# Kernel tuning notes

Measured on AMD Instinct MI355X. Metric: run time of the kernel, lower is better.

Reference implementation:

```python
import jax, jax.numpy as jnp
import numpy as np

N = 50000          # nodes
E = 800000         # edges (avg degree 16)
F_IN = 128         # node_feat_dim
HEADS = 4
HID = 64           # hidden_dim (per head)
LAT = 64           # latent_dim
N_EC = 8           # num_edge_classes
SLOPE = 0.2        # GATConv default negative_slope


def setup_inputs() -> dict:
    key = jax.random.key(0)
    ks = jax.random.split(key, 20)
    s = 0.05
    inp = {
        "x": jax.random.normal(ks[0], (N, F_IN), jnp.float32),
        "edge_index": jax.random.randint(ks[1], (2, E), 0, N, jnp.int32),
        # conv1: GATConv(F_IN, HID, heads=HEADS)
        "W1": jax.random.normal(ks[2], (F_IN, HEADS * HID), jnp.float32) * s,
        "att_src1": jax.random.normal(ks[3], (HEADS, HID), jnp.float32) * s,
        "att_dst1": jax.random.normal(ks[4], (HEADS, HID), jnp.float32) * s,
        "b1": jnp.zeros((HEADS * HID,), jnp.float32),
        # conv2: GATConv(HEADS*HID, LAT, heads=1)
        "W2": jax.random.normal(ks[5], (HEADS * HID, LAT), jnp.float32) * s,
        "att_src2": jax.random.normal(ks[6], (1, LAT), jnp.float32) * s,
        "att_dst2": jax.random.normal(ks[7], (1, LAT), jnp.float32) * s,
        "b2": jnp.zeros((LAT,), jnp.float32),
        # decode_nodes: Linear(LAT, F_IN)
        "Wn": jax.random.normal(ks[8], (LAT, F_IN), jnp.float32) * s,
        "bn": jnp.zeros((F_IN,), jnp.float32),
        # decode_edges: Linear(2*LAT, HID) -> ReLU -> Linear(HID, N_EC)
        "We1": jax.random.normal(ks[9], (2 * LAT, HID), jnp.float32) * s,
        "be1": jnp.zeros((HID,), jnp.float32),
        "We2": jax.random.normal(ks[10], (HID, N_EC), jnp.float32) * s,
        "be2": jnp.zeros((N_EC,), jnp.float32),
    }
    return inp


def _gat_conv(x, src, dst, W, att_src, att_dst, b, heads, out_ch):
    """PyG-style GATConv: message src->dst, segment-softmax over incoming edges."""
    n = x.shape[0]
    h = (x @ W).reshape(n, heads, out_ch)          # [N, H, C]
    a_s = (h * att_src).sum(-1)                     # [N, H]
    a_d = (h * att_dst).sum(-1)                     # [N, H]
    alpha = jax.nn.leaky_relu(a_s[src] + a_d[dst], SLOPE)   # [E', H]
    amax = jax.ops.segment_max(alpha, dst, num_segments=n)  # stable softmax
    alpha = jnp.exp(alpha - amax[dst])
    denom = jax.ops.segment_sum(alpha, dst, num_segments=n)
    alpha = alpha / (denom[dst] + 1e-16)
    out = jax.ops.segment_sum(h[src] * alpha[:, :, None], dst, num_segments=n)
    return out.reshape(n, heads * out_ch) + b


def reference(x, edge_index, W1, att_src1, att_dst1, b1, W2, att_src2, att_dst2,
              b2, Wn, bn, We1, be1, We2, be2):
    n = x.shape[0]
    loop = jnp.arange(n, dtype=edge_index.dtype)
    # PyG GATConv adds self-loops by default
    src = jnp.concatenate([edge_index[0], loop])
    dst = jnp.concatenate([edge_index[1], loop])

    h = jax.nn.relu(_gat_conv(x, src, dst, W1, att_src1, att_dst1, b1, HEADS, HID))
    z = _gat_conv(h, src, dst, W2, att_src2, att_dst2, b2, 1, LAT)

    recon_x = z @ Wn + bn
    # edge decode uses the ORIGINAL edge_index (no self-loops)
    edge_z = jnp.concatenate([z[edge_index[0]], z[edge_index[1]]], axis=-1)
    recon_edge_logits = jax.nn.relu(edge_z @ We1 + be1) @ We2 + be2
    return (recon_x, recon_edge_logits)
```

## Files before the change

### kernel.cpp

```cpp
#include <hip/hip_runtime.h>

#define N_NODES 50000
#define N_EDGES 800000
#define F_IN    128
#define HEADS   4
#define HID     64
#define LAT     64
#define N_EC    8
#define SLOPE   0.2f
#define NBUCKET 196
#define PLANE   ((size_t)N_NODES * 128)
#define PLANEU  ((size_t)N_NODES * 64)

typedef __attribute__((ext_vector_type(8))) short bf16x8;
typedef __attribute__((ext_vector_type(4))) float f32x4;

__device__ __forceinline__ float lrelu(float x) { return x > 0.f ? x : SLOPE * x; }
__device__ __forceinline__ float4 operator+(float4 a, float4 b) { return make_float4(a.x+b.x, a.y+b.y, a.z+b.z, a.w+b.w); }
__device__ __forceinline__ float4 lrelu4(float4 a) { return make_float4(lrelu(a.x), lrelu(a.y), lrelu(a.z), lrelu(a.w)); }
__device__ __forceinline__ float4 exp4(float4 a) { return make_float4(__expf(a.x), __expf(a.y), __expf(a.z), __expf(a.w)); }

__device__ __forceinline__ unsigned short f2bf(float f) {
    union { float f; unsigned u; } a; a.f = f;
    unsigned r = a.u + 0x7fffu + ((a.u >> 16) & 1u);
    return (unsigned short)(r >> 16);
}
__device__ __forceinline__ unsigned pack2bf(float x, float y) {
    return (unsigned)f2bf(x) | ((unsigned)f2bf(y) << 16);
}
__device__ __forceinline__ float2 bf2f2(unsigned u) {
    union { unsigned q; float f; } a, b;
    a.q = u << 16; b.q = u & 0xffff0000u;
    return make_float2(a.f, b.f);
}

__global__ __launch_bounds__(256) void bucket_count_kernel(const int* __restrict__ ei,
                                                           int* __restrict__ bcnt) {
    __shared__ int h[NBUCKET];
    int tid = threadIdx.x;
    for (int i = tid; i < NBUCKET; i += 256) h[i] = 0;
    __syncthreads();
    int beg = blockIdx.x * 4096;
    int end = min(beg + 4096, N_EDGES);
    for (int e = beg + tid; e < end; e += 256)
        atomicAdd(&h[ei[N_EDGES + e] >> 8], 1);
    __syncthreads();
    for (int i = tid; i < NBUCKET; i += 256)
        if (h[i]) atomicAdd(&bcnt[i], h[i]);
}

__global__ __launch_bounds__(256) void scan_buckets_kernel(const int* __restrict__ bcnt,
                                                           int* __restrict__ bbase,
                                                           int* __restrict__ bcur,
                                                           int* __restrict__ row_start) {
    __shared__ int sh[NBUCKET + 1];
    int tid = threadIdx.x;
    if (tid < NBUCKET) { sh[tid] = bcnt[tid]; bcur[tid] = 0; }
    __syncthreads();
    if (tid == 0) {
        int a = 0;
        for (int i = 0; i < NBUCKET; i++) { int t = sh[i]; sh[i] = a; a += t; }
        sh[NBUCKET] = a;
        row_start[N_NODES] = N_EDGES;
    }
    __syncthreads();
    if (tid <= NBUCKET) bbase[tid] = sh[tid];
}

__global__ __launch_bounds__(256) void coarse_scatter_kernel(const int* __restrict__ ei,
                                                             const int* __restrict__ bbase,
                                                             int* __restrict__ bcur,
                                                             uint2* __restrict__ coarse) {
    __shared__ int h[NBUCKET];
    __shared__ int base[NBUCKET];
    int tid = threadIdx.x;
    for (int i = tid; i < NBUCKET; i += 256) h[i] = 0;
    __syncthreads();
    int beg = blockIdx.x * 4096;
    int w0_[16], o_[16], b_[16];
#pragma unroll
    for (int k = 0; k < 16; k++) {
        int e = beg + k * 256 + tid;
        b_[k] = -1;
        if (e < N_EDGES) {
            int s = ei[e], d = ei[N_EDGES + e];
            int bk = d >> 8;
            b_[k] = bk;
            w0_[k] = s | ((d & 255) << 16);
            o_[k] = e;
            atomicAdd(&h[bk], 1);
        }
    }
    __syncthreads();
    for (int i = tid; i < NBUCKET; i += 256) {
        int c = h[i];
        base[i] = c ? atomicAdd(&bcur[i], c) : 0;
        h[i] = 0;
    }
    __syncthreads();
#pragma unroll
    for (int k = 0; k < 16; k++) {
        if (b_[k] >= 0) {
            int r = atomicAdd(&h[b_[k]], 1);
            coarse[bbase[b_[k]] + base[b_[k]] + r] = make_uint2((unsigned)w0_[k], (unsigned)o_[k]);
        }
    }
}

__global__ __launch_bounds__(256) void fine_pass_kernel(const uint2* __restrict__ coarse,
                                                        const int* __restrict__ bbase,
                                                        const float4* __restrict__ as4,
                                                        const float4* __restrict__ ad4,
                                                        int* __restrict__ esrc,
                                                        float4* __restrict__ alpha4,
                                                        uint2* __restrict__ edges2,
                                                        int* __restrict__ row_start) {
    int bucket = blockIdx.x;
    int tid = threadIdx.x;
    int lo = bbase[bucket], hi = bbase[bucket + 1];
    __shared__ int h[256];
    __shared__ int wsum[4];
    __shared__ int cur[256];
    h[tid] = 0;
    __syncthreads();
    for (int p = lo + tid; p < hi; p += 256)
        atomicAdd(&h[(coarse[p].x >> 16) & 0xff], 1);
    __syncthreads();
    int v = h[tid];
    int lane = tid & 63, w = tid >> 6;
    int incl = v;
#pragma unroll
    for (int off = 1; off < 64; off <<= 1) {
        int t = __shfl_up(incl, off, 64);
        if (lane >= off) incl += t;
    }
    if (lane == 63) wsum[w] = incl;
    __syncthreads();
    if (tid == 0) {
        int a = 0;
#pragma unroll
        for (int i = 0; i < 4; i++) { int t = wsum[i]; wsum[i] = a; a += t; }
    }
    __syncthreads();
    int excl = incl - v + wsum[w];
    int node = bucket * 256 + tid;
    if (node < N_NODES) row_start[node] = lo + excl;
    cur[tid] = lo + excl;
    __syncthreads();
    for (int p = lo + tid; p < hi; p += 256) {
        uint2 r = coarse[p];
        int dl = (r.x >> 16) & 0xff;
        int s = r.x & 0xffff;
        int d = bucket * 256 + dl;
        int pos = atomicAdd(&cur[dl], 1);
        esrc[pos] = s;
        edges2[pos] = make_uint2((unsigned)(s | (d << 16)), r.y);
        alpha4[pos] = exp4(lrelu4(as4[s] + ad4[d]));
    }
}

__global__ void watt_kernel(const float* __restrict__ W1, const float* __restrict__ as_,
                            const float* __restrict__ ad_, float* __restrict__ watt) {
    int idx = blockIdx.x * blockDim.x + threadIdx.x;
    if (idx >= 128 * 8) return;
    int k = idx >> 3, j = idx & 7;
    int h = j & 3;
    const float* av = (j < 4) ? as_ : ad_;
    float sum = 0.f;
    for (int c = 0; c < 64; c++) sum += W1[k * 256 + h * 64 + c] * av[h * 64 + c];
    watt[k * 8 + j] = sum;
}

__global__ void build_wts_kernel(const float* __restrict__ W1, const float* __restrict__ W2,
                                 const float* __restrict__ Wn, const float* __restrict__ We1,
                                 const float* __restrict__ We2,
                                 unsigned short* __restrict__ Bt1, unsigned short* __restrict__ Bt2,
                                 unsigned short* __restrict__ Btd, unsigned short* __restrict__ Bte) {
    int idx = blockIdx.x * blockDim.x + threadIdx.x;
    if (idx < 256 * 128) {
        int n = idx >> 7, k = idx & 127;
        Bt1[idx] = f2bf(W1[k * 256 + n]);
    }
    if (idx < 64 * 256) {
        int n = idx >> 8, k = idx & 255;
        Bt2[idx] = f2bf(W2[k * 64 + n]);
    }
    if (idx < 256 * 64) {
        int n = idx >> 6, k = idx & 63;
        float v;
        if (n < 128) v = Wn[k * 128 + n];
        else {
            int nn = n - 128;
            v = (nn < 64) ? We1[k * 64 + nn] : We1[(64 + k) * 64 + (nn - 64)];
        }
        Btd[idx] = f2bf(v);
    }
    if (idx < 16 * 64) {
        int n = idx >> 6, k = idx & 63;
        Bte[idx] = (n < 8) ? f2bf(We2[k * 8 + n]) : (unsigned short)0;
    }
}

__global__ __launch_bounds__(256) void asad_kernel(const float* __restrict__ x,
                                                   const float* __restrict__ watt,
                                                   float4* __restrict__ as4,
                                                   float4* __restrict__ ad4,
                                                   unsigned* __restrict__ xb) {
    int wid = (blockIdx.x * blockDim.x + threadIdx.x) >> 6;
    int lane = threadIdx.x & 63;
    if (wid >= N_NODES) return;
    float2 xv = *reinterpret_cast<const float2*>(&x[(size_t)wid * 128 + lane * 2]);
    xb[(size_t)wid * 64 + lane] = pack2bf(xv.x, xv.y);
    float p[8];
    const float* w0 = &watt[(2 * lane) * 8];
    const float* w1 = &watt[(2 * lane + 1) * 8];
#pragma unroll
    for (int j = 0; j < 8; j++) p[j] = fmaf(xv.x, w0[j], xv.y * w1[j]);
#pragma unroll
    for (int off = 32; off; off >>= 1)
#pragma unroll
        for (int j = 0; j < 8; j++) p[j] += __shfl_xor(p[j], off, 64);
    if (lane == 0) {
        as4[wid] = make_float4(p[0], p[1], p[2], p[3]);
        ad4[wid] = make_float4(p[4], p[5], p[6], p[7]);
    }
}

__global__ __launch_bounds__(256) void agg4x_acc_kernel(const unsigned short* __restrict__ xb,
                                                        const float4* __restrict__ as4,
                                                        const float4* __restrict__ ad4,
                                                        const int* __restrict__ row_start,
                                                        const int* __restrict__ esrc,
                                                        const float4* __restrict__ alpha4,
                                                        unsigned* __restrict__ xaggb) {
    int wid = (blockIdx.x * blockDim.x + threadIdx.x) >> 6;
    int lane = threadIdx.x & 63;
    if (wid >= N_NODES) return;
    int beg = __builtin_amdgcn_readfirstlane(row_start[wid]);
    int end = __builtin_amdgcn_readfirstlane(row_start[wid + 1]);
    float4 adn = ad4[wid];
    float4 e_self = exp4(lrelu4(as4[wid] + adn));
    float4 den = e_self;
    float2 xv = bf2f2(*reinterpret_cast<const unsigned*>(&xb[(size_t)wid * 128 + lane * 2]));
    float2 acc0 = make_float2(e_self.x * xv.x, e_self.x * xv.y);
    float2 acc1 = make_float2(e_self.y * xv.x, e_self.y * xv.y);
    float2 acc2 = make_float2(e_self.z * xv.x, e_self.z * xv.y);
    float2 acc3 = make_float2(e_self.w * xv.x, e_self.w * xv.y);
    int j = beg;
    for (; j + 1 < end; j += 2) {
        float4 ea = alpha4[j];
        int sa = esrc[j];
        float4 eb = alpha4[j + 1];
        int sb = esrc[j + 1];
        float2 va = bf2f2(*reinterpret_cast<const unsigned*>(&xb[(size_t)sa * 128 + lane * 2]));
        float2 vb = bf2f2(*reinterpret_cast<const unsigned*>(&xb[(size_t)sb * 128 + lane * 2]));
        acc0.x = fmaf(ea.x, va.x, acc0.x); acc0.y = fmaf(ea.x, va.y, acc0.y);
        acc1.x = fmaf(ea.y, va.x, acc1.x); acc1.y = fmaf(ea.y, va.y, acc1.y);
        acc2.x = fmaf(ea.z, va.x, acc2.x); acc2.y = fmaf(ea.z, va.y, acc2.y);
        acc3.x = fmaf(ea.w, va.x, acc3.x); acc3.y = fmaf(ea.w, va.y, acc3.y);
        den = den + ea;
        acc0.x = fmaf(eb.x, vb.x, acc0.x); acc0.y = fmaf(eb.x, vb.y, acc0.y);
        acc1.x = fmaf(eb.y, vb.x, acc1.x); acc1.y = fmaf(eb.y, vb.y, acc1.y);
        acc2.x = fmaf(eb.z, vb.x, acc2.x); acc2.y = fmaf(eb.z, vb.y, acc2.y);
        acc3.x = fmaf(eb.w, vb.x, acc3.x); acc3.y = fmaf(eb.w, vb.y, acc3.y);
        den = den + eb;
    }
    if (j < end) {
        float4 ea = alpha4[j];
        int sa = esrc[j];
        float2 va = bf2f2(*reinterpret_cast<const unsigned*>(&xb[(size_t)sa * 128 + lane * 2]));
        acc0.x = fmaf(ea.x, va.x, acc0.x); acc0.y = fmaf(ea.x, va.y, acc0.y);
        acc1.x = fmaf(ea.y, va.x, acc1.x); acc1.y = fmaf(ea.y, va.y, acc1.y);
        acc2.x = fmaf(ea.z, va.x, acc2.x); acc2.y = fmaf(ea.z, va.y, acc2.y);
        acc3.x = fmaf(ea.w, va.x, acc3.x); acc3.y = fmaf(ea.w, va.y, acc3.y);
        den = den + ea;
    }
    float i0 = 1.f / (den.x + 1e-16f);
    float i1 = 1.f / (den.y + 1e-16f);
    float i2 = 1.f / (den.z + 1e-16f);
    float i3 = 1.f / (den.w + 1e-16f);
    size_t base = (size_t)wid * 64 + lane;
    xaggb[0 * PLANEU + base] = pack2bf(acc0.x * i0, acc0.y * i0);
    xaggb[1 * PLANEU + base] = pack2bf(acc1.x * i1, acc1.y * i1);
    xaggb[2 * PLANEU + base] = pack2bf(acc2.x * i2, acc2.y * i2);
    xaggb[3 * PLANEU + base] = pack2bf(acc3.x * i3, acc3.y * i3);
}


template <int K>
__global__ __launch_bounds__(256) void mfma_gemm1_kernel(const unsigned short* __restrict__ A,
                                                         int lda, long aPlane,
                                                         const unsigned short* __restrict__ Bt,
                                                         const float* __restrict__ bias,
                                                         unsigned short* __restrict__ C, int ldc,
                                                         int M) {
    int tid = threadIdx.x;
    int w = tid >> 6, l = tid & 63;
    int bcol = blockIdx.y * 64;
    A += (size_t)blockIdx.y * aPlane;
    int row_a = blockIdx.x * 64 + w * 16 + (l & 15);
    int kq = (l >> 4) * 8;
    bool aval = row_a < M;
    const unsigned short* Arow = A + (size_t)row_a * lda;
    f32x4 acc[4] = {};
#pragma unroll
    for (int kb = 0; kb < K / 32; kb++) {
        int k0 = kb * 32 + kq;
        bf16x8 a = {};
        if (aval) a = *reinterpret_cast<const bf16x8*>(&Arow[k0]);
#pragma unroll
        for (int nb = 0; nb < 4; nb++) {
            bf16x8 b = *reinterpret_cast<const bf16x8*>(
                &Bt[(size_t)(bcol + nb * 16 + (l & 15)) * K + k0]);
            acc[nb] = __builtin_amdgcn_mfma_f32_16x16x32_bf16(a, b, acc[nb], 0, 0, 0);
        }
    }
    int orow = blockIdx.x * 64 + w * 16 + (l >> 4) * 4;
#pragma unroll
    for (int nb = 0; nb < 4; nb++) {
        int col = bcol + nb * 16 + (l & 15);
        float bb = bias[col];
#pragma unroll
        for (int r = 0; r < 4; r++) {
            int row = orow + r;
            if (row < M) C[(size_t)row * ldc + col] = f2bf(fmaxf(acc[nb][r] + bb, 0.f));
        }
    }
}

__global__ __launch_bounds__(256) void mfma_gemm2_kernel(const unsigned short* __restrict__ A,
                                                         const unsigned short* __restrict__ Bt,
                                                         const float* __restrict__ att_src,
                                                         const float* __restrict__ att_dst,
                                                         unsigned short* __restrict__ h2b,
                                                         float* __restrict__ as_,
                                                         float* __restrict__ ad_, int M) {
    int tid = threadIdx.x;
    int w = tid >> 6, l = tid & 63;
    int row_a = blockIdx.x * 64 + w * 16 + (l & 15);
    int kq = (l >> 4) * 8;
    bool aval = row_a < M;
    const unsigned short* Arow = A + (size_t)row_a * 256;
    f32x4 acc[4] = {};
#pragma unroll
    for (int kb = 0; kb < 8; kb++) {
        int k0 = kb * 32 + kq;
        bf16x8 a = {};
        if (aval) a = *reinterpret_cast<const bf16x8*>(&Arow[k0]);
#pragma unroll
        for (int nb = 0; nb < 4; nb++) {
            bf16x8 b = *reinterpret_cast<const bf16x8*>(
                &Bt[(size_t)(nb * 16 + (l & 15)) * 256 + k0]);
            acc[nb] = __builtin_amdgcn_mfma_f32_16x16x32_bf16(a, b, acc[nb], 0, 0, 0);
        }
    }
    int orow = blockIdx.x * 64 + w * 16 + (l >> 4) * 4;
    float ps[4] = {}, pd[4] = {};
#pragma unroll
    for (int nb = 0; nb < 4; nb++) {
        int col = nb * 16 + (l & 15);
        float s = att_src[col], dd = att_dst[col];
#pragma unroll
        for (int r = 0; r < 4; r++) {
            float v = acc[nb][r];
            ps[r] = fmaf(v, s, ps[r]);
            pd[r] = fmaf(v, dd, pd[r]);
            int row = orow + r;
            if (row < M) h2b[(size_t)row * 64 + col] = f2bf(v);
        }
    }
#pragma unroll
    for (int off = 1; off <= 8; off <<= 1)
#pragma unroll
        for (int r = 0; r < 4; r++) {
            ps[r] += __shfl_xor(ps[r], off, 64);
            pd[r] += __shfl_xor(pd[r], off, 64);
        }
    if ((l & 15) == 0) {
#pragma unroll
        for (int r = 0; r < 4; r++) {
            int row = orow + r;
            if (row < M) { as_[row] = ps[r]; ad_[row] = pd[r]; }
        }
    }
}

__global__ __launch_bounds__(256) void mfma_gemm_decode_kernel(const unsigned short* __restrict__ zb,
                                                               const unsigned short* __restrict__ Btd,
                                                               const float* __restrict__ bn,
                                                               float* __restrict__ recon_x,
                                                               unsigned short* __restrict__ PQb,
                                                               int M) {
    int tid = threadIdx.x;
    int w = tid >> 6, l = tid & 63;
    int bcol = blockIdx.y * 64;
    int row_a = blockIdx.x * 64 + w * 16 + (l & 15);
    int kq = (l >> 4) * 8;
    bool aval = row_a < M;
    const unsigned short* Arow = zb + (size_t)row_a * 64;
    f32x4 acc[4] = {};
#pragma unroll
    for (int kb = 0; kb < 2; kb++) {
        int k0 = kb * 32 + kq;
        bf16x8 a = {};
        if (aval) a = *reinterpret_cast<const bf16x8*>(&Arow[k0]);
#pragma unroll
        for (int nb = 0; nb < 4; nb++) {
            bf16x8 b = *reinterpret_cast<const bf16x8*>(
                &Btd[(size_t)(bcol + nb * 16 + (l & 15)) * 64 + k0]);
            acc[nb] = __builtin_amdgcn_mfma_f32_16x16x32_bf16(a, b, acc[nb], 0, 0, 0);
        }
    }
    int orow = blockIdx.x * 64 + w * 16 + (l >> 4) * 4;
#pragma unroll
    for (int nb = 0; nb < 4; nb++) {
        int col = bcol + nb * 16 + (l & 15);
        if (col < 128) {
            float bb = bn[col];
#pragma unroll
            for (int r = 0; r < 4; r++) {
                int row = orow + r;
                if (row < M) recon_x[(size_t)row * 128 + col] = acc[nb][r] + bb;
            }
        } else {
#pragma unroll
            for (int r = 0; r < 4; r++) {
                int row = orow + r;
                if (row < M) PQb[(size_t)row * 128 + (col - 128)] = f2bf(acc[nb][r]);
            }
        }
    }
}

__global__ void alpha1_kernel(const uint2* __restrict__ edges2,
                              const float* __restrict__ as_, const float* __restrict__ ad_,
                              float* __restrict__ alpha1) {
    int p = blockIdx.x * blockDim.x + threadIdx.x;
    if (p < N_EDGES) {
        unsigned w0 = edges2[p].x;
        alpha1[p] = __expf(lrelu(as_[w0 & 0xffff] + ad_[w0 >> 16]));
    }
}

__global__ __launch_bounds__(256) void agg1_acc_kernel(const unsigned short* __restrict__ h2b,
                                                       const float* __restrict__ as_,
                                                       const float* __restrict__ ad_,
                                                       const int* __restrict__ row_start,
                                                       const int* __restrict__ esrc,
                                                       const float* __restrict__ alpha1,
                                                       const float* __restrict__ bias,
                                                       unsigned* __restrict__ zb) {
    int wid = (blockIdx.x * blockDim.x + threadIdx.x) >> 6;
    int lane = threadIdx.x & 63;
    if (wid >= N_NODES) return;
    int g = lane >> 5;
    int c = lane & 31;
    int beg = __builtin_amdgcn_readfirstlane(row_start[wid]);
    int end = __builtin_amdgcn_readfirstlane(row_start[wid + 1]);
    float adn = ad_[wid];
    float e_self = __expf(lrelu(as_[wid] + adn));
    float den = (g == 0) ? e_self : 0.f;
    float2 hv = bf2f2(*reinterpret_cast<const unsigned*>(&h2b[(size_t)wid * 64 + 2 * c]));
    float2 acc = (g == 0) ? make_float2(e_self * hv.x, e_self * hv.y)
                          : make_float2(0.f, 0.f);
    for (int j = beg; j < end; j += 2) {
        float a0 = alpha1[j];
        int s0 = esrc[j];
        float a1 = 0.f;
        int s1 = s0;
        if (j + 1 < end) { a1 = alpha1[j + 1]; s1 = esrc[j + 1]; }
        float e = g ? a1 : a0;
        int s = g ? s1 : s0;
        float2 v = bf2f2(*reinterpret_cast<const unsigned*>(&h2b[(size_t)s * 64 + 2 * c]));
        acc.x = fmaf(e, v.x, acc.x);
        acc.y = fmaf(e, v.y, acc.y);
        den += e;
    }
    den += __shfl_xor(den, 32, 64);
    acc.x += __shfl_xor(acc.x, 32, 64);
    acc.y += __shfl_xor(acc.y, 32, 64);
    if (g == 0) {
        float inv = 1.f / (den + 1e-16f);
        float2 bb = *reinterpret_cast<const float2*>(&bias[2 * c]);
        zb[(size_t)wid * 32 + c] = pack2bf(acc.x * inv + bb.x, acc.y * inv + bb.y);
    }
}

#define ED_BLOCKS 2048
__device__ __forceinline__ bf16x8 make_t(uint4 up, uint4 uq, float4 ba, float4 bb) {
    float2 p0 = bf2f2(up.x), p1 = bf2f2(up.y), p2 = bf2f2(up.z), p3 = bf2f2(up.w);
    float2 q0 = bf2f2(uq.x), q1 = bf2f2(uq.y), q2 = bf2f2(uq.z), q3 = bf2f2(uq.w);
    unsigned r0 = pack2bf(fmaxf(p0.x + q0.x + ba.x, 0.f), fmaxf(p0.y + q0.y + ba.y, 0.f));
    unsigned r1 = pack2bf(fmaxf(p1.x + q1.x + ba.z, 0.f), fmaxf(p1.y + q1.y + ba.w, 0.f));
    unsigned r2 = pack2bf(fmaxf(p2.x + q2.x + bb.x, 0.f), fmaxf(p2.y + q2.y + bb.y, 0.f));
    unsigned r3 = pack2bf(fmaxf(p3.x + q3.x + bb.z, 0.f), fmaxf(p3.y + q3.y + bb.w, 0.f));
    union { uint4 u; bf16x8 v; } c;
    c.u = make_uint4(r0, r1, r2, r3);
    return c.v;
}

__global__ __launch_bounds__(256) void mfma_edge_decode_kernel(const unsigned short* __restrict__ PQb,
                                                               const uint2* __restrict__ edges2,
                                                               const float* __restrict__ be1,
                                                               const unsigned short* __restrict__ Bte,
                                                               const float* __restrict__ be2,
                                                               float* __restrict__ out) {
    int tid = threadIdx.x;
    int l = tid & 63;
    int col = l & 15;
    int kq = (l >> 4) * 8;
    bf16x8 b0 = *reinterpret_cast<const bf16x8*>(&Bte[col * 64 + kq]);
    bf16x8 b1 = *reinterpret_cast<const bf16x8*>(&Bte[col * 64 + 32 + kq]);
    float4 ba0 = *reinterpret_cast<const float4*>(&be1[kq]);
    float4 bb0 = *reinterpret_cast<const float4*>(&be1[kq + 4]);
    float4 ba1 = *reinterpret_cast<const float4*>(&be1[32 + kq]);
    float4 bb1 = *reinterpret_cast<const float4*>(&be1[32 + kq + 4]);
    float bout = (col < 8) ? be2[col] : 0.f;
    int rbase = (l >> 4) * 4;

    int wgid = (blockIdx.x * blockDim.x + tid) >> 6;
    const int nwaves = ED_BLOCKS * 4;
    const int ngroups = N_EDGES / 16;
    for (int g = wgid; g < ngroups; g += nwaves) {
        int base = g * 16;
        uint2 t2 = edges2[base + col];
        int s = t2.x & 0xffff, d = t2.x >> 16;
        const unsigned short* Pr = &PQb[(size_t)s * 128];
        const unsigned short* Qr = &PQb[(size_t)d * 128 + 64];
        uint4 up0 = *reinterpret_cast<const uint4*>(&Pr[kq]);
        uint4 uq0 = *reinterpret_cast<const uint4*>(&Qr[kq]);
        uint4 up1 = *reinterpret_cast<const uint4*>(&Pr[32 + kq]);
        uint4 uq1 = *reinterpret_cast<const uint4*>(&Qr[32 + kq]);
        bf16x8 a0 = make_t(up0, uq0, ba0, bb0);
        bf16x8 a1 = make_t(up1, uq1, ba1, bb1);
        f32x4 acc = {};
        acc = __builtin_amdgcn_mfma_f32_16x16x32_bf16(a0, b0, acc, 0, 0, 0);
        acc = __builtin_amdgcn_mfma_f32_16x16x32_bf16(a1, b1, acc, 0, 0, 0);
        if (col < 8) {
#pragma unroll
            for (int r = 0; r < 4; r++) {
                int o = edges2[base + rbase + r].y;
                out[(size_t)o * 8 + col] = acc[r] + bout;
            }
        }
    }
}

extern "C" void kernel_launch(void* const* d_in, const int* in_sizes, int n_in,
                              void* d_out, int out_size, void* d_ws, size_t ws_size,
                              hipStream_t stream) {
    const float* x        = (const float*)d_in[0];
    const int*   ei       = (const int*)d_in[1];
    const float* W1       = (const float*)d_in[2];
    const float* att_src1 = (const float*)d_in[3];
    const float* att_dst1 = (const float*)d_in[4];
    const float* b1       = (const float*)d_in[5];
    const float* W2       = (const float*)d_in[6];
    const float* att_src2 = (const float*)d_in[7];
    const float* att_dst2 = (const float*)d_in[8];
    const float* b2       = (const float*)d_in[9];
    const float* Wn       = (const float*)d_in[10];
    const float* bn       = (const float*)d_in[11];
    const float* We1      = (const float*)d_in[12];
    const float* be1      = (const float*)d_in[13];
    const float* We2      = (const float*)d_in[14];
    const float* be2      = (const float*)d_in[15];

    char* ws = (char*)d_ws;
    size_t off = 0;
    auto alloc = [&](size_t bytes) {
        void* p = ws + off;
        off += (bytes + 255) & ~(size_t)255;
        return p;
    };
    int*   bcnt      = (int*)alloc((size_t)NBUCKET * 4);
    int*   bbase     = (int*)alloc((size_t)(NBUCKET + 1) * 4);
    int*   bcur      = (int*)alloc((size_t)NBUCKET * 4);
    int*   row_start = (int*)alloc((size_t)(N_NODES + 1) * 4);
    uint2* coarse    = (uint2*)alloc((size_t)N_EDGES * 8);
    uint2* edges2    = (uint2*)alloc((size_t)N_EDGES * 8);
    int*   esrc      = (int*)alloc((size_t)N_EDGES * 4);
    float* watt      = (float*)alloc((size_t)128 * 8 * 4);
    float* as1       = (float*)alloc((size_t)N_NODES * 4 * 4);
    float* ad1       = (float*)alloc((size_t)N_NODES * 4 * 4);
    unsigned* xb     = (unsigned*)alloc((size_t)N_NODES * 64 * 4);
    float* alpha4    = (float*)alloc((size_t)N_EDGES * 4 * 4);
    unsigned* xaggb  = (unsigned*)alloc((size_t)4 * PLANEU * 4);
    unsigned short* houtb = (unsigned short*)alloc((size_t)N_NODES * 256 * 2);
    unsigned* h2b    = (unsigned*)alloc((size_t)N_NODES * 32 * 4);
    float* as2       = (float*)alloc((size_t)N_NODES * 4);
    float* ad2       = (float*)alloc((size_t)N_NODES * 4);
    float* alpha1    = (float*)alloc((size_t)N_EDGES * 4);
    unsigned* zb     = (unsigned*)alloc((size_t)N_NODES * 32 * 4);
    unsigned short* PQb = (unsigned short*)alloc((size_t)N_NODES * 128 * 2);
    unsigned short* Bt1 = (unsigned short*)alloc((size_t)256 * 128 * 2);
    unsigned short* Bt2 = (unsigned short*)alloc((size_t)64 * 256 * 2);
    unsigned short* Btd = (unsigned short*)alloc((size_t)256 * 64 * 2);
    unsigned short* Bte = (unsigned short*)alloc((size_t)16 * 64 * 2);

    float* recon_x = (float*)d_out;
    float* recon_e = (float*)d_out + (size_t)N_NODES * F_IN;

    const int ablocks = (N_EDGES + 4095) / 4096;

    hipMemsetAsync(bcnt, 0, (size_t)NBUCKET * 4, stream);
    bucket_count_kernel<<<ablocks, 256, 0, stream>>>(ei, bcnt);
    scan_buckets_kernel<<<1, 256, 0, stream>>>(bcnt, bbase, bcur, row_start);
    watt_kernel<<<4, 256, 0, stream>>>(W1, att_src1, att_dst1, watt);
    build_wts_kernel<<<128, 256, 0, stream>>>(W1, W2, Wn, We1, We2, Bt1, Bt2, Btd, Bte);
    asad_kernel<<<(N_NODES * 64 + 255) / 256, 256, 0, stream>>>(x, watt, (float4*)as1,
                                                                (float4*)ad1, xb);
    coarse_scatter_kernel<<<ablocks, 256, 0, stream>>>(ei, bbase, bcur, coarse);
    fine_pass_kernel<<<NBUCKET, 256, 0, stream>>>(coarse, bbase, (const float4*)as1,
                                                  (const float4*)ad1, esrc, (float4*)alpha4,
                                                  edges2, row_start);

    agg4x_acc_kernel<<<(N_NODES * 64 + 255) / 256, 256, 0, stream>>>(
        (const unsigned short*)xb, (const float4*)as1, (const float4*)ad1, row_start, esrc,
        (const float4*)alpha4, xaggb);
    dim3 gc1((N_NODES + 63) / 64, 4);
    mfma_gemm1_kernel<128><<<gc1, 256, 0, stream>>>(
        (const unsigned short*)xaggb, 128, (long)PLANE, Bt1, b1, houtb, 256, N_NODES);

    mfma_gemm2_kernel<<<(N_NODES + 63) / 64, 256, 0, stream>>>(
        houtb, Bt2, att_src2, att_dst2, (unsigned short*)h2b, as2, ad2, N_NODES);
    alpha1_kernel<<<(N_EDGES + 255) / 256, 256, 0, stream>>>(edges2, as2, ad2, alpha1);
    agg1_acc_kernel<<<(N_NODES * 64 + 255) / 256, 256, 0, stream>>>(
        (const unsigned short*)h2b, as2, ad2, row_start, esrc, alpha1, b2, zb);

    dim3 gdec((N_NODES + 63) / 64, 4);
    mfma_gemm_decode_kernel<<<gdec, 256, 0, stream>>>(
        (const unsigned short*)zb, Btd, bn, recon_x, PQb, N_NODES);

    mfma_edge_decode_kernel<<<ED_BLOCKS, 256, 0, stream>>>(PQb, edges2, be1, Bte, be2, recon_e);
}
```

Measured before the change: 305.4 us.

## Pack edge records with fp16 alphas and use deterministic per-block bucket offsets

Merges esrc, edges2 and the fp32 alpha4 array into one 16-byte edge record holding src/dst, original edge id and four fp16 attention weights. The layer-1 aggregation then reads one record per edge, and its loop is unrolled by four. Bucket counting now writes per-block histograms that a single-block scan turns into global offsets, replacing the global atomics and the memset. The weight-prep kernels are merged into one launch. The cost is fp16 precision on the unnormalised exp weights, which could overflow for large logits, plus a serial column scan of a 196x196 table in one block.

```diff
diff --git a/kernel.cpp b/kernel.cpp
--- a/kernel.cpp
+++ b/kernel.cpp
@@ -1,4 +1,5 @@
 #include <hip/hip_runtime.h>
+#include <hip/hip_fp16.h>
 
 #define N_NODES 50000
 #define N_EDGES 800000
@@ -9,6 +10,7 @@
 #define N_EC    8
 #define SLOPE   0.2f
 #define NBUCKET 196
+#define NABLK   196
 #define PLANE   ((size_t)N_NODES * 128)
 #define PLANEU  ((size_t)N_NODES * 64)
 
@@ -33,9 +35,17 @@
     a.q = u << 16; b.q = u & 0xffff0000u;
     return make_float2(a.f, b.f);
 }
+__device__ __forceinline__ unsigned pack2h(float x, float y) {
+    __half2 h = __floats2half2_rn(x, y);
+    return *reinterpret_cast<unsigned*>(&h);
+}
+__device__ __forceinline__ float2 unpack2h(unsigned u) {
+    __half2 h = *reinterpret_cast<__half2*>(&u);
+    return __half22float2(h);
+}
 
 __global__ __launch_bounds__(256) void bucket_count_kernel(const int* __restrict__ ei,
-                                                           int* __restrict__ bcnt) {
+                                                           int* __restrict__ hist) {
     __shared__ int h[NBUCKET];
     int tid = threadIdx.x;
     for (int i = tid; i < NBUCKET; i += 256) h[i] = 0;
@@ -46,30 +56,41 @@
         atomicAdd(&h[ei[N_EDGES + e] >> 8], 1);
     __syncthreads();
     for (int i = tid; i < NBUCKET; i += 256)
-        if (h[i]) atomicAdd(&bcnt[i], h[i]);
-}
-
-__global__ __launch_bounds__(256) void scan_buckets_kernel(const int* __restrict__ bcnt,
+        hist[blockIdx.x * NBUCKET + i] = h[i];
+}
+
+__global__ __launch_bounds__(256) void scan_buckets_kernel(int* __restrict__ hist,
                                                            int* __restrict__ bbase,
-                                                           int* __restrict__ bcur,
                                                            int* __restrict__ row_start) {
-    __shared__ int sh[NBUCKET + 1];
-    int tid = threadIdx.x;
-    if (tid < NBUCKET) { sh[tid] = bcnt[tid]; bcur[tid] = 0; }
+    __shared__ int colsum[NBUCKET];
+    int tid = threadIdx.x;
+    if (tid < NBUCKET) {
+        int acc = 0;
+        for (int b = 0; b < NABLK; b++) {
+            int idx = b * NBUCKET + tid;
+            int v = hist[idx];
+            hist[idx] = acc;
+            acc += v;
+        }
+        colsum[tid] = acc;
+    }
     __syncthreads();
     if (tid == 0) {
         int a = 0;
-        for (int i = 0; i < NBUCKET; i++) { int t = sh[i]; sh[i] = a; a += t; }
-        sh[NBUCKET] = a;
+        for (int i = 0; i < NBUCKET; i++) { int t = colsum[i]; colsum[i] = a; a += t; }
         row_start[N_NODES] = N_EDGES;
     }
     __syncthreads();
-    if (tid <= NBUCKET) bbase[tid] = sh[tid];
+    if (tid < NBUCKET) {
+        int base = colsum[tid];
+        bbase[tid] = base;
+        for (int b = 0; b < NABLK; b++) hist[b * NBUCKET + tid] += base;
+    }
+    if (tid == 0) bbase[NBUCKET] = N_EDGES;
 }
 
 __global__ __launch_bounds__(256) void coarse_scatter_kernel(const int* __restrict__ ei,
-                                                             const int* __restrict__ bbase,
-                                                             int* __restrict__ bcur,
+                                                             const int* __restrict__ basetab,
                                                              uint2* __restrict__ coarse) {
     __shared__ int h[NBUCKET];
     __shared__ int base[NBUCKET];
@@ -93,8 +114,7 @@
     }
     __syncthreads();
     for (int i = tid; i < NBUCKET; i += 256) {
-        int c = h[i];
-        base[i] = c ? atomicAdd(&bcur[i], c) : 0;
+        base[i] = basetab[blockIdx.x * NBUCKET + i];
         h[i] = 0;
     }
     __syncthreads();
@@ -102,7 +122,7 @@
     for (int k = 0; k < 16; k++) {
         if (b_[k] >= 0) {
             int r = atomicAdd(&h[b_[k]], 1);
-            coarse[bbase[b_[k]] + base[b_[k]] + r] = make_uint2((unsigned)w0_[k], (unsigned)o_[k]);
+            coarse[base[b_[k]] + r] = make_uint2((unsigned)w0_[k], (unsigned)o_[k]);
         }
     }
 }
@@ -111,9 +131,7 @@
                                                         const int* __restrict__ bbase,
                                                         const float4* __restrict__ as4,
                                                         const float4* __restrict__ ad4,
-                                                        int* __restrict__ esrc,
-                                                        float4* __restrict__ alpha4,
-                                                        uint2* __restrict__ edges2,
+                                                        uint4* __restrict__ edges,
                                                         int* __restrict__ row_start) {
     int bucket = blockIdx.x;
     int tid = threadIdx.x;
@@ -152,30 +170,20 @@
         int dl = (r.x >> 16) & 0xff;
         int s = r.x & 0xffff;
         int d = bucket * 256 + dl;
+        float4 al = exp4(lrelu4(as4[s] + ad4[d]));
         int pos = atomicAdd(&cur[dl], 1);
-        esrc[pos] = s;
-        edges2[pos] = make_uint2((unsigned)(s | (d << 16)), r.y);
-        alpha4[pos] = exp4(lrelu4(as4[s] + ad4[d]));
-    }
-}
-
-__global__ void watt_kernel(const float* __restrict__ W1, const float* __restrict__ as_,
-                            const float* __restrict__ ad_, float* __restrict__ watt) {
-    int idx = blockIdx.x * blockDim.x + threadIdx.x;
-    if (idx >= 128 * 8) return;
-    int k = idx >> 3, j = idx & 7;
-    int h = j & 3;
-    const float* av = (j < 4) ? as_ : ad_;
-    float sum = 0.f;
-    for (int c = 0; c < 64; c++) sum += W1[k * 256 + h * 64 + c] * av[h * 64 + c];
-    watt[k * 8 + j] = sum;
-}
-
-__global__ void build_wts_kernel(const float* __restrict__ W1, const float* __restrict__ W2,
-                                 const float* __restrict__ Wn, const float* __restrict__ We1,
-                                 const float* __restrict__ We2,
-                                 unsigned short* __restrict__ Bt1, unsigned short* __restrict__ Bt2,
-                                 unsigned short* __restrict__ Btd, unsigned short* __restrict__ Bte) {
+        edges[pos] = make_uint4((unsigned)(s | (d << 16)), r.y,
+                                pack2h(al.x, al.y), pack2h(al.z, al.w));
+    }
+}
+
+__global__ void wts_kernel(const float* __restrict__ W1, const float* __restrict__ W2,
+                           const float* __restrict__ Wn, const float* __restrict__ We1,
+                           const float* __restrict__ We2,
+                           const float* __restrict__ as_, const float* __restrict__ ad_,
+                           float* __restrict__ watt,
+                           unsigned short* __restrict__ Bt1, unsigned short* __restrict__ Bt2,
+                           unsigned short* __restrict__ Btd, unsigned short* __restrict__ Bte) {
     int idx = blockIdx.x * blockDim.x + threadIdx.x;
     if (idx < 256 * 128) {
         int n = idx >> 7, k = idx & 127;
@@ -198,6 +206,14 @@
     if (idx < 16 * 64) {
         int n = idx >> 6, k = idx & 63;
         Bte[idx] = (n < 8) ? f2bf(We2[k * 8 + n]) : (unsigned short)0;
+    }
+    if (idx < 128 * 8) {
+        int k = idx >> 3, j = idx & 7;
+        int h = j & 3;
+        const float* av = (j < 4) ? as_ : ad_;
+        float sum = 0.f;
+        for (int c = 0; c < 64; c++) sum += W1[k * 256 + h * 64 + c] * av[h * 64 + c];
+        watt[k * 8 + j] = sum;
     }
 }
 
@@ -226,12 +242,11 @@
     }
 }
 
-__global__ __launch_bounds__(256) void agg4x_acc_kernel(const unsigned short* __restrict__ xb,
+__global__ __launch_bounds__(256) void agg4x_acc_kernel(const unsigned* __restrict__ xb,
                                                         const float4* __restrict__ as4,
                                                         const float4* __restrict__ ad4,
                                                         const int* __restrict__ row_start,
-                                                        const int* __restrict__ esrc,
-                                                        const float4* __restrict__ alpha4,
+                                                        const uint4* __restrict__ edges,
                                                         unsigned* __restrict__ xaggb) {
     int wid = (blockIdx.x * blockDim.x + threadIdx.x) >> 6;
     int lane = threadIdx.x & 63;
@@ -241,40 +256,42 @@
     float4 adn = ad4[wid];
     float4 e_self = exp4(lrelu4(as4[wid] + adn));
     float4 den = e_self;
-    float2 xv = bf2f2(*reinterpret_cast<const unsigned*>(&xb[(size_t)wid * 128 + lane * 2]));
+    float2 xv = bf2f2(xb[(size_t)wid * 64 + lane]);
     float2 acc0 = make_float2(e_self.x * xv.x, e_self.x * xv.y);
     float2 acc1 = make_float2(e_self.y * xv.x, e_self.y * xv.y);
     float2 acc2 = make_float2(e_self.z * xv.x, e_self.z * xv.y);
     float2 acc3 = make_float2(e_self.w * xv.x, e_self.w * xv.y);
+
+#define EDGE_ACC(rec, vu)                                                     \
+    {                                                                         \
+        float2 a01 = unpack2h((rec).z);                                       \
+        float2 a23 = unpack2h((rec).w);                                       \
+        float2 vv = bf2f2(vu);                                                \
+        acc0.x = fmaf(a01.x, vv.x, acc0.x); acc0.y = fmaf(a01.x, vv.y, acc0.y); \
+        acc1.x = fmaf(a01.y, vv.x, acc1.x); acc1.y = fmaf(a01.y, vv.y, acc1.y); \
+        acc2.x = fmaf(a23.x, vv.x, acc2.x); acc2.y = fmaf(a23.x, vv.y, acc2.y); \
+        acc3.x = fmaf(a23.y, vv.x, acc3.x); acc3.y = fmaf(a23.y, vv.y, acc3.y); \
+        den.x += a01.x; den.y += a01.y; den.z += a23.x; den.w += a23.y;       \
+    }
+
     int j = beg;
-    for (; j + 1 < end; j += 2) {
-        float4 ea = alpha4[j];
-        int sa = esrc[j];
-        float4 eb = alpha4[j + 1];
-        int sb = esrc[j + 1];
-        float2 va = bf2f2(*reinterpret_cast<const unsigned*>(&xb[(size_t)sa * 128 + lane * 2]));
-        float2 vb = bf2f2(*reinterpret_cast<const unsigned*>(&xb[(size_t)sb * 128 + lane * 2]));
-        acc0.x = fmaf(ea.x, va.x, acc0.x); acc0.y = fmaf(ea.x, va.y, acc0.y);
-        acc1.x = fmaf(ea.y, va.x, acc1.x); acc1.y = fmaf(ea.y, va.y, acc1.y);
-        acc2.x = fmaf(ea.z, va.x, acc2.x); acc2.y = fmaf(ea.z, va.y, acc2.y);
-        acc3.x = fmaf(ea.w, va.x, acc3.x); acc3.y = fmaf(ea.w, va.y, acc3.y);
-        den = den + ea;
-        acc0.x = fmaf(eb.x, vb.x, acc0.x); acc0.y = fmaf(eb.x, vb.y, acc0.y);
-        acc1.x = fmaf(eb.y, vb.x, acc1.x); acc1.y = fmaf(eb.y, vb.y, acc1.y);
-        acc2.x = fmaf(eb.z, vb.x, acc2.x); acc2.y = fmaf(eb.z, vb.y, acc2.y);
-        acc3.x = fmaf(eb.w, vb.x, acc3.x); acc3.y = fmaf(eb.w, vb.y, acc3.y);
-        den = den + eb;
-    }
-    if (j < end) {
-        float4 ea = alpha4[j];
-        int sa = esrc[j];
-        float2 va = bf2f2(*reinterpret_cast<const unsigned*>(&xb[(size_t)sa * 128 + lane * 2]));
-        acc0.x = fmaf(ea.x, va.x, acc0.x); acc0.y = fmaf(ea.x, va.y, acc0.y);
-        acc1.x = fmaf(ea.y, va.x, acc1.x); acc1.y = fmaf(ea.y, va.y, acc1.y);
-        acc2.x = fmaf(ea.z, va.x, acc2.x); acc2.y = fmaf(ea.z, va.y, acc2.y);
-        acc3.x = fmaf(ea.w, va.x, acc3.x); acc3.y = fmaf(ea.w, va.y, acc3.y);
-        den = den + ea;
-    }
+    for (; j + 3 < end; j += 4) {
+        uint4 r0 = edges[j], r1 = edges[j + 1], r2 = edges[j + 2], r3 = edges[j + 3];
+        unsigned v0 = xb[(size_t)(r0.x & 0xffff) * 64 + lane];
+        unsigned v1 = xb[(size_t)(r1.x & 0xffff) * 64 + lane];
+        unsigned v2 = xb[(size_t)(r2.x & 0xffff) * 64 + lane];
+        unsigned v3 = xb[(size_t)(r3.x & 0xffff) * 64 + lane];
+        EDGE_ACC(r0, v0);
+        EDGE_ACC(r1, v1);
+        EDGE_ACC(r2, v2);
+        EDGE_ACC(r3, v3);
+    }
+    for (; j < end; j++) {
+        uint4 r = edges[j];
+        unsigned v = xb[(size_t)(r.x & 0xffff) * 64 + lane];
+        EDGE_ACC(r, v);
+    }
+#undef EDGE_ACC
     float i0 = 1.f / (den.x + 1e-16f);
     float i1 = 1.f / (den.y + 1e-16f);
     float i2 = 1.f / (den.z + 1e-16f);
@@ -432,21 +449,21 @@
     }
 }
 
-__global__ void alpha1_kernel(const uint2* __restrict__ edges2,
+__global__ void alpha1_kernel(const uint4* __restrict__ edges,
                               const float* __restrict__ as_, const float* __restrict__ ad_,
                               float* __restrict__ alpha1) {
     int p = blockIdx.x * blockDim.x + threadIdx.x;
     if (p < N_EDGES) {
-        unsigned w0 = edges2[p].x;
+        unsigned w0 = edges[p].x;
         alpha1[p] = __expf(lrelu(as_[w0 & 0xffff] + ad_[w0 >> 16]));
     }
 }
 
-__global__ __launch_bounds__(256) void agg1_acc_kernel(const unsigned short* __restrict__ h2b,
+__global__ __launch_bounds__(256) void agg1_acc_kernel(const unsigned* __restrict__ h2b,
                                                        const float* __restrict__ as_,
                                                        const float* __restrict__ ad_,
                                                        const int* __restrict__ row_start,
-                                                       const int* __restrict__ esrc,
+                                                       const uint4* __restrict__ edges,
                                                        const float* __restrict__ alpha1,
                                                        const float* __restrict__ bias,
                                                        unsigned* __restrict__ zb) {
@@ -460,18 +477,18 @@
     float adn = ad_[wid];
     float e_self = __expf(lrelu(as_[wid] + adn));
     float den = (g == 0) ? e_self : 0.f;
-    float2 hv = bf2f2(*reinterpret_cast<const unsigned*>(&h2b[(size_t)wid * 64 + 2 * c]));
+    float2 hv = bf2f2(h2b[(size_t)wid * 32 + c]);
     float2 acc = (g == 0) ? make_float2(e_self * hv.x, e_self * hv.y)
                           : make_float2(0.f, 0.f);
     for (int j = beg; j < end; j += 2) {
         float a0 = alpha1[j];
-        int s0 = esrc[j];
+        int s0 = edges[j].x & 0xffff;
         float a1 = 0.f;
         int s1 = s0;
-        if (j + 1 < end) { a1 = alpha1[j + 1]; s1 = esrc[j + 1]; }
+        if (j + 1 < end) { a1 = alpha1[j + 1]; s1 = edges[j + 1].x & 0xffff; }
         float e = g ? a1 : a0;
         int s = g ? s1 : s0;
-        float2 v = bf2f2(*reinterpret_cast<const unsigned*>(&h2b[(size_t)s * 64 + 2 * c]));
+        float2 v = bf2f2(h2b[(size_t)s * 32 + c]);
         acc.x = fmaf(e, v.x, acc.x);
         acc.y = fmaf(e, v.y, acc.y);
         den += e;
@@ -500,7 +517,7 @@
 }
 
 __global__ __launch_bounds__(256) void mfma_edge_decode_kernel(const unsigned short* __restrict__ PQb,
-                                                               const uint2* __restrict__ edges2,
+                                                               const uint4* __restrict__ edges,
                                                                const float* __restrict__ be1,
                                                                const unsigned short* __restrict__ Bte,
                                                                const float* __restrict__ be2,
@@ -523,8 +540,8 @@
     const int ngroups = N_EDGES / 16;
     for (int g = wgid; g < ngroups; g += nwaves) {
         int base = g * 16;
-        uint2 t2 = edges2[base + col];
-        int s = t2.x & 0xffff, d = t2.x >> 16;
+        unsigned ex = edges[base + col].x;
+        int s = ex & 0xffff, d = ex >> 16;
         const unsigned short* Pr = &PQb[(size_t)s * 128];
         const unsigned short* Qr = &PQb[(size_t)d * 128 + 64];
         uint4 up0 = *reinterpret_cast<const uint4*>(&Pr[kq]);
@@ -539,7 +556,7 @@
         if (col < 8) {
 #pragma unroll
             for (int r = 0; r < 4; r++) {
-                int o = edges2[base + rbase + r].y;
+                int o = edges[base + rbase + r].y;
                 out[(size_t)o * 8 + col] = acc[r] + bout;
             }
         }
@@ -573,18 +590,15 @@
         off += (bytes + 255) & ~(size_t)255;
         return p;
     };
-    int*   bcnt      = (int*)alloc((size_t)NBUCKET * 4);
+    int*   hist      = (int*)alloc((size_t)NABLK * NBUCKET * 4);
     int*   bbase     = (int*)alloc((size_t)(NBUCKET + 1) * 4);
-    int*   bcur      = (int*)alloc((size_t)NBUCKET * 4);
     int*   row_start = (int*)alloc((size_t)(N_NODES + 1) * 4);
     uint2* coarse    = (uint2*)alloc((size_t)N_EDGES * 8);
-    uint2* edges2    = (uint2*)alloc((size_t)N_EDGES * 8);
-    int*   esrc      = (int*)alloc((size_t)N_EDGES * 4);
+    uint4* edges     = (uint4*)alloc((size_t)N_EDGES * 16);
     float* watt      = (float*)alloc((size_t)128 * 8 * 4);
     float* as1       = (float*)alloc((size_t)N_NODES * 4 * 4);
     float* ad1       = (float*)alloc((size_t)N_NODES * 4 * 4);
     unsigned* xb     = (unsigned*)alloc((size_t)N_NODES * 64 * 4);
-    float* alpha4    = (float*)alloc((size_t)N_EDGES * 4 * 4);
     unsigned* xaggb  = (unsigned*)alloc((size_t)4 * PLANEU * 4);
     unsigned short* houtb = (unsigned short*)alloc((size_t)N_NODES * 256 * 2);
     unsigned* h2b    = (unsigned*)alloc((size_t)N_NODES * 32 * 4);
@@ -601,36 +615,31 @@
     float* recon_x = (float*)d_out;
     float* recon_e = (float*)d_out + (size_t)N_NODES * F_IN;
 
-    const int ablocks = (N_EDGES + 4095) / 4096;
-
-    hipMemsetAsync(bcnt, 0, (size_t)NBUCKET * 4, stream);
-    bucket_count_kernel<<<ablocks, 256, 0, stream>>>(ei, bcnt);
-    scan_buckets_kernel<<<1, 256, 0, stream>>>(bcnt, bbase, bcur, row_start);
-    watt_kernel<<<4, 256, 0, stream>>>(W1, att_src1, att_dst1, watt);
-    build_wts_kernel<<<128, 256, 0, stream>>>(W1, W2, Wn, We1, We2, Bt1, Bt2, Btd, Bte);
+    bucket_count_kernel<<<NABLK, 256, 0, stream>>>(ei, hist);
+    scan_buckets_kernel<<<1, 256, 0, stream>>>(hist, bbase, row_start);
+    wts_kernel<<<128, 256, 0, stream>>>(W1, W2, Wn, We1, We2, att_src1, att_dst1,
+                                        watt, Bt1, Bt2, Btd, Bte);
     asad_kernel<<<(N_NODES * 64 + 255) / 256, 256, 0, stream>>>(x, watt, (float4*)as1,
                                                                 (float4*)ad1, xb);
-    coarse_scatter_kernel<<<ablocks, 256, 0, stream>>>(ei, bbase, bcur, coarse);
+    coarse_scatter_kernel<<<NABLK, 256, 0, stream>>>(ei, hist, coarse);
     fine_pass_kernel<<<NBUCKET, 256, 0, stream>>>(coarse, bbase, (const float4*)as1,
-                                                  (const float4*)ad1, esrc, (float4*)alpha4,
-                                                  edges2, row_start);
+                                                  (const float4*)ad1, edges, row_start);
 
     agg4x_acc_kernel<<<(N_NODES * 64 + 255) / 256, 256, 0, stream>>>(
-        (const unsigned short*)xb, (const float4*)as1, (const float4*)ad1, row_start, esrc,
-        (const float4*)alpha4, xaggb);
+        xb, (const float4*)as1, (const float4*)ad1, row_start, edges, xaggb);
     dim3 gc1((N_NODES + 63) / 64, 4);
     mfma_gemm1_kernel<128><<<gc1, 256, 0, stream>>>(
         (const unsigned short*)xaggb, 128, (long)PLANE, Bt1, b1, houtb, 256, N_NODES);
 
     mfma_gemm2_kernel<<<(N_NODES + 63) / 64, 256, 0, stream>>>(
         houtb, Bt2, att_src2, att_dst2, (unsigned short*)h2b, as2, ad2, N_NODES);
-    alpha1_kernel<<<(N_EDGES + 255) / 256, 256, 0, stream>>>(edges2, as2, ad2, alpha1);
+    alpha1_kernel<<<(N_EDGES + 255) / 256, 256, 0, stream>>>(edges, as2, ad2, alpha1);
     agg1_acc_kernel<<<(N_NODES * 64 + 255) / 256, 256, 0, stream>>>(
-        (const unsigned short*)h2b, as2, ad2, row_start, esrc, alpha1, b2, zb);
+        h2b, as2, ad2, row_start, edges, alpha1, b2, zb);
 
     dim3 gdec((N_NODES + 63) / 64, 4);
     mfma_gemm_decode_kernel<<<gdec, 256, 0, stream>>>(
         (const unsigned short*)zb, Btd, bn, recon_x, PQb, N_NODES);
 
-    mfma_edge_decode_kernel<<<ED_BLOCKS, 256, 0, stream>>>(PQb, edges2, be1, Bte, be2, recon_e);
-}
+    mfma_edge_decode_kernel<<<ED_BLOCKS, 256, 0, stream>>>(PQb, edges, be1, Bte, be2, recon_e);
+}
```

Measured after the change: 306.7 us. Within noise of the previous version (+0.4%).
